# Performance work log

Measured on AMD Instinct MI355X. Metric: run time of the kernel, lower is better.

Reference implementation:

```python
import jax, jax.numpy as jnp
import numpy as np


def setup_inputs() -> dict:
    key = jax.random.key(0)
    k1, k2 = jax.random.split(key)
    B, D, C = 4096, 128, 64
    score = jax.random.normal(k1, (B, D), dtype=jnp.float32)
    target = jax.random.randint(k2, (B,), 0, C, dtype=jnp.int64)
    alpha = jnp.full((1,), 9.0, dtype=jnp.float32)  # learned margin param
    return {"score": score, "target": target, "alpha": alpha}


def _pairwise_dist(score):
    # squared euclidean: ||xi||^2 + ||xj||^2 - 2 xi.xj, clamped at 0, then sqrt
    mag = jnp.sum(score * score, axis=1)            # [B]
    d2 = mag[:, None] + mag[None, :] - 2.0 * (score @ score.T)
    d2 = jnp.maximum(d2, 0.0)
    # safe sqrt (diagonal is exactly 0; avoid nan grads)
    safe = jnp.where(d2 > 0.0, d2, 1.0)
    return jnp.where(d2 > 0.0, jnp.sqrt(safe), 0.0)  # [B, B]


def reference(score, target, alpha):
    target = target.reshape(-1)
    B = score.shape[0]
    dist = _pairwise_dist(score)                    # [B, B]
    diff = target[:, None] != target[None, :]       # [B, B] negative-pair mask
    # per-anchor sum over negatives of exp(alpha - dist); diagonal excluded (same label)
    nes = jnp.sum(jnp.where(diff, jnp.exp(alpha[0] - dist), 0.0), axis=1)  # [B]
    l_n = jnp.log(nes[:, None] + nes[None, :])      # [B, B]
    # positive pairs i<j with equal labels
    upper = jnp.triu(jnp.ones((B, B), dtype=bool), k=1)
    pos = (~diff) & upper
    terms = jnp.where(pos, jax.nn.relu(l_n + dist) ** 2, 0.0)
    counter = jnp.sum(pos).astype(score.dtype)
    return jnp.sum(terms) / (2.0 * counter)
```

## Files before the change

### kernel.cpp

```cpp
#include <hip/hip_runtime.h>
#include <math.h>

#define BN 4096
#define DD 128
#define NCLS 64
#define PSPLIT 16
#define NPOSB (NCLS * PSPLIT)
#define NJB 32

typedef __attribute__((ext_vector_type(8))) short short8;
typedef __attribute__((ext_vector_type(4))) float f32x4;

__device__ __forceinline__ unsigned short f2bf(float f) {
    unsigned int u = __float_as_uint(f);
    u += 0x7FFFu + ((u >> 16) & 1u);
    return (unsigned short)(u >> 16);
}

__device__ __forceinline__ void gload_lds16(const void* g, void* l) {
    __builtin_amdgcn_global_load_lds(
        (const __attribute__((address_space(1))) unsigned int*)g,
        (__attribute__((address_space(3))) unsigned int*)l, 16, 0, 0);
}


__global__ __launch_bounds__(256)
void prep_bucket_kernel(const float* __restrict__ score, const int* __restrict__ target,
                        unsigned short* __restrict__ sbf, float* __restrict__ mag,
                        int* __restrict__ cls_cnt, int* __restrict__ cls_start,
                        int* __restrict__ cls_list) {
    __shared__ int hist[NCLS];
    __shared__ int offs[NCLS];
    const int tid = threadIdx.x;
    if (blockIdx.x < BN / 4) {
        int row  = blockIdx.x * 4 + (tid >> 6);
        int lane = tid & 63;
        float2 v = *reinterpret_cast<const float2*>(score + (size_t)row * DD + lane * 2);
        float s = v.x * v.x + v.y * v.y;
        #pragma unroll
        for (int off = 32; off; off >>= 1) s += __shfl_xor(s, off);
        ushort2 u; u.x = f2bf(v.x); u.y = f2bf(v.y);
        *reinterpret_cast<ushort2*>(sbf + (size_t)row * DD + lane * 2) = u;
        if (lane == 0) mag[row] = s;
    } else {
        if (tid < NCLS) hist[tid] = 0;
        __syncthreads();
        for (int i = tid; i < BN; i += 256) atomicAdd(&hist[target[i]], 1);
        __syncthreads();
        if (tid == 0) {
            int run = 0;
            for (int c = 0; c < NCLS; ++c) {
                cls_cnt[c] = hist[c];
                cls_start[c] = run;
                offs[c] = run;
                run += hist[c];
            }
        }
        __syncthreads();
        for (int i = tid; i < BN; i += 256) {
            int p = atomicAdd(&offs[target[i]], 1);
            cls_list[p] = i;
        }
    }
}

__global__ __launch_bounds__(256)
void nes_kernel(const unsigned short* __restrict__ sbf, const int* __restrict__ target,
                const float* __restrict__ alphap, const float* __restrict__ mag,
                float* __restrict__ nes_part) {
    const int ib = blockIdx.x, jb = blockIdx.y;
    if (jb < ib) return;
    __shared__ __align__(16) unsigned short lds[2 * 128 * 128];
    __shared__ float rowsum[2][128];
    __shared__ float colsum[2][128];
    const int tid = threadIdx.x;
    const int w = tid >> 6, lane = tid & 63;
    const int lhi = lane >> 4, llo = lane & 15;
    const int i0 = ib * 128, j0 = jb * 128;
    const bool diag = (ib == jb);

    #pragma unroll
    for (int t = 0; t < 8; ++t) {
        int rl = w * 32 + t * 4 + lhi;
        int ch = llo ^ (rl & 7);
        gload_lds16(sbf + (size_t)(i0 + rl) * DD + ch * 8, lds + (w * 32 + t * 4) * 128);
        if (!diag)
            gload_lds16(sbf + (size_t)(j0 + rl) * DD + ch * 8,
                        lds + 128 * 128 + (w * 32 + t * 4) * 128);
    }
    __syncthreads();

    const unsigned short* bbase = diag ? lds : (lds + 128 * 128);
    const int wr = w >> 1, wc = w & 1;
    f32x4 acc[4][4] = {};
    #pragma unroll
    for (int kk = 0; kk < 4; ++kk) {
        short8 a[4], b[4];
        #pragma unroll
        for (int m = 0; m < 4; ++m) {
            int r = wr * 64 + m * 16 + llo;
            int ch = (kk * 4 + lhi) ^ (r & 7);
            a[m] = *reinterpret_cast<const short8*>(lds + r * 128 + ch * 8);
        }
        #pragma unroll
        for (int n = 0; n < 4; ++n) {
            int r = wc * 64 + n * 16 + llo;
            int ch = (kk * 4 + lhi) ^ (r & 7);
            b[n] = *reinterpret_cast<const short8*>(bbase + r * 128 + ch * 8);
        }
        #pragma unroll
        for (int m = 0; m < 4; ++m)
            #pragma unroll
            for (int n = 0; n < 4; ++n)
                acc[m][n] = __builtin_amdgcn_mfma_f32_16x16x32_bf16(a[m], b[n], acc[m][n], 0, 0, 0);
    }

    const float alpha = alphap[0];
    float mj[4]; int tj[4];
    #pragma unroll
    for (int n = 0; n < 4; ++n) {
        int j = j0 + wc * 64 + n * 16 + llo;
        mj[n] = mag[j]; tj[n] = target[j];
    }
    float cs[4] = {0.f, 0.f, 0.f, 0.f};
    #pragma unroll
    for (int m = 0; m < 4; ++m) {
        #pragma unroll
        for (int rg = 0; rg < 4; ++rg) {
            int li = wr * 64 + m * 16 + lhi * 4 + rg;
            int i = i0 + li;
            float mi = mag[i];
            int ti = target[i];
            float rs = 0.f;
            #pragma unroll
            for (int n = 0; n < 4; ++n) {
                float d2 = fmaxf(mi + mj[n] - 2.0f * acc[m][n][rg], 0.0f);
                float dist = sqrtf(d2);
                float e = (ti != tj[n]) ? __expf(alpha - dist) : 0.0f;
                rs += e;
                cs[n] += e;
            }
            rs += __shfl_xor(rs, 1);
            rs += __shfl_xor(rs, 2);
            rs += __shfl_xor(rs, 4);
            rs += __shfl_xor(rs, 8);
            if (llo == 0) rowsum[wc][li] = rs;
        }
    }
    #pragma unroll
    for (int n = 0; n < 4; ++n) {
        cs[n] += __shfl_xor(cs[n], 16);
        cs[n] += __shfl_xor(cs[n], 32);
        if (lhi == 0) colsum[wr][wc * 64 + n * 16 + llo] = cs[n];
    }
    __syncthreads();
    if (tid < 128) {
        nes_part[(size_t)(i0 + tid) * NJB + jb] = rowsum[0][tid] + rowsum[1][tid];
        if (!diag)
            nes_part[(size_t)(j0 + tid) * NJB + ib] = colsum[0][tid] + colsum[1][tid];
    }
}

__global__ __launch_bounds__(256)
void pos_kernel(const float* __restrict__ score, const float* __restrict__ nes_part,
                const int* __restrict__ cls_cnt, const int* __restrict__ cls_start,
                const int* __restrict__ cls_list,
                float* __restrict__ part_sum, unsigned int* __restrict__ part_cnt) {
    __shared__ float ssum[4];
    __shared__ unsigned int scnt[4];
    const int c = blockIdx.x;
    const int n = cls_cnt[c], s0 = cls_start[c];
    const int tid = threadIdx.x;
    const int grp = tid >> 4, llo = tid & 15;
    const int g0 = blockIdx.y * 16 + grp;
    const int nG = 16 * PSPLIT;
    const int nn = n * n;
    float s = 0.f;
    unsigned int cc = 0;
    for (int p = g0; p < nn; p += nG) {
        int a = p / n, b = p - a * n;
        if (b <= a) continue;
        int i = cls_list[s0 + a], j = cls_list[s0 + b];
        const float4* ra = reinterpret_cast<const float4*>(score + (size_t)i * DD) + llo * 2;
        const float4* rb = reinterpret_cast<const float4*>(score + (size_t)j * DD) + llo * 2;
        float4 x0 = ra[0], x1 = ra[1];
        float4 y0 = rb[0], y1 = rb[1];
        float dx;
        float d2 = 0.f;
        dx = x0.x - y0.x; d2 += dx * dx;
        dx = x0.y - y0.y; d2 += dx * dx;
        dx = x0.z - y0.z; d2 += dx * dx;
        dx = x0.w - y0.w; d2 += dx * dx;
        dx = x1.x - y1.x; d2 += dx * dx;
        dx = x1.y - y1.y; d2 += dx * dx;
        dx = x1.z - y1.z; d2 += dx * dx;
        dx = x1.w - y1.w; d2 += dx * dx;
        float2 pi = *reinterpret_cast<const float2*>(nes_part + (size_t)i * NJB + llo * 2);
        float2 pj = *reinterpret_cast<const float2*>(nes_part + (size_t)j * NJB + llo * 2);
        float ni = pi.x + pi.y;
        float nj = pj.x + pj.y;
        #pragma unroll
        for (int off = 1; off < 16; off <<= 1) {
            d2 += __shfl_xor(d2, off);
            ni += __shfl_xor(ni, off);
            nj += __shfl_xor(nj, off);
        }
        if (llo == 0) {
            float dist = sqrtf(d2);
            float t = __logf(ni + nj) + dist;
            if (t > 0.f) s += t * t;
            cc++;
        }
    }
    #pragma unroll
    for (int off = 1; off < 64; off <<= 1) {
        s += __shfl_xor(s, off);
        cc += __shfl_xor(cc, off);
    }
    if ((tid & 63) == 0) { ssum[tid >> 6] = s; scnt[tid >> 6] = cc; }
    __syncthreads();
    if (tid == 0) {
        int bid = blockIdx.y * NCLS + blockIdx.x;
        part_sum[bid] = ssum[0] + ssum[1] + ssum[2] + ssum[3];
        part_cnt[bid] = scnt[0] + scnt[1] + scnt[2] + scnt[3];
    }
}

__global__ __launch_bounds__(256)
void finalize_kernel(const float* __restrict__ part_sum,
                     const unsigned int* __restrict__ part_cnt,
                     float* __restrict__ out) {
    __shared__ float fs[4];
    __shared__ unsigned int fc[4];
    int tid = threadIdx.x;
    float s = 0.f;
    unsigned int c = 0;
    #pragma unroll
    for (int k = 0; k < NPOSB / 256; ++k) {
        s += part_sum[k * 256 + tid];
        c += part_cnt[k * 256 + tid];
    }
    #pragma unroll
    for (int off = 1; off < 64; off <<= 1) {
        s += __shfl_xor(s, off);
        c += __shfl_xor(c, off);
    }
    if ((tid & 63) == 0) { fs[tid >> 6] = s; fc[tid >> 6] = c; }
    __syncthreads();
    if (tid == 0) {
        float S = fs[0] + fs[1] + fs[2] + fs[3];
        float C = (float)(fc[0] + fc[1] + fc[2] + fc[3]);
        out[0] = S / (2.0f * C);
    }
}

extern "C" void kernel_launch(void* const* d_in, const int* in_sizes, int n_in,
                              void* d_out, int out_size, void* d_ws, size_t ws_size,
                              hipStream_t stream) {
    const float* score  = (const float*)d_in[0];
    const int*   target = (const int*)d_in[1];
    const float* alpha  = (const float*)d_in[2];
    float* out = (float*)d_out;

    unsigned short* sbf = (unsigned short*)d_ws;
    float* mag      = (float*)((char*)d_ws + (size_t)BN * DD * 2);
    float* nes_part = mag + BN;
    float* part_sum = nes_part + (size_t)BN * NJB;
    unsigned int* part_cnt = (unsigned int*)(part_sum + NPOSB);
    int* cls_cnt   = (int*)(part_cnt + NPOSB);
    int* cls_start = cls_cnt + NCLS;
    int* cls_list  = cls_start + NCLS;

    prep_bucket_kernel<<<BN / 4 + 1, 256, 0, stream>>>(score, target, sbf, mag,
                                                       cls_cnt, cls_start, cls_list);
    dim3 g(BN / 128, BN / 128);
    nes_kernel<<<g, 256, 0, stream>>>(sbf, target, alpha, mag, nes_part);
    pos_kernel<<<dim3(NCLS, PSPLIT), 256, 0, stream>>>(score, nes_part,
                                                       cls_cnt, cls_start, cls_list,
                                                       part_sum, part_cnt);
    finalize_kernel<<<1, 256, 0, stream>>>(part_sum, part_cnt, out);
}
```

Before: 109.8 us.

## Fuse all stages into one persistent kernel with grid-wide barriers

```diff
diff --git a/kernel.cpp b/kernel.cpp
--- a/kernel.cpp
+++ b/kernel.cpp
@@ -4,8 +4,9 @@
 #define BN 4096
 #define DD 128
 #define NCLS 64
-#define PSPLIT 16
-#define NPOSB (NCLS * PSPLIT)
+#define NT 32
+#define NTILES (NT * (NT + 1) / 2)
+#define NBLK 256
 #define NJB 32
 
 typedef __attribute__((ext_vector_type(8))) short short8;
@@ -23,234 +24,248 @@
         (__attribute__((address_space(3))) unsigned int*)l, 16, 0, 0);
 }
 
+__device__ __forceinline__ void grid_barrier(unsigned int* bar, int idx) {
+    __syncthreads();
+    if (threadIdx.x == 0) {
+        __threadfence();
+        atomicAdd(&bar[idx], 1u);
+        while (__hip_atomic_load(&bar[idx], __ATOMIC_ACQUIRE, __HIP_MEMORY_SCOPE_AGENT) < NBLK)
+            __builtin_amdgcn_s_sleep(2);
+    }
+    __syncthreads();
+    __threadfence();
+}
+
 
 __global__ __launch_bounds__(256)
-void prep_bucket_kernel(const float* __restrict__ score, const int* __restrict__ target,
-                        unsigned short* __restrict__ sbf, float* __restrict__ mag,
-                        int* __restrict__ cls_cnt, int* __restrict__ cls_start,
-                        int* __restrict__ cls_list) {
-    __shared__ int hist[NCLS];
-    __shared__ int offs[NCLS];
-    const int tid = threadIdx.x;
-    if (blockIdx.x < BN / 4) {
-        int row  = blockIdx.x * 4 + (tid >> 6);
-        int lane = tid & 63;
-        float2 v = *reinterpret_cast<const float2*>(score + (size_t)row * DD + lane * 2);
-        float s = v.x * v.x + v.y * v.y;
-        #pragma unroll
-        for (int off = 32; off; off >>= 1) s += __shfl_xor(s, off);
-        ushort2 u; u.x = f2bf(v.x); u.y = f2bf(v.y);
-        *reinterpret_cast<ushort2*>(sbf + (size_t)row * DD + lane * 2) = u;
-        if (lane == 0) mag[row] = s;
-    } else {
-        if (tid < NCLS) hist[tid] = 0;
-        __syncthreads();
-        for (int i = tid; i < BN; i += 256) atomicAdd(&hist[target[i]], 1);
-        __syncthreads();
-        if (tid == 0) {
-            int run = 0;
-            for (int c = 0; c < NCLS; ++c) {
-                cls_cnt[c] = hist[c];
-                cls_start[c] = run;
-                offs[c] = run;
-                run += hist[c];
-            }
-        }
-        __syncthreads();
-        for (int i = tid; i < BN; i += 256) {
-            int p = atomicAdd(&offs[target[i]], 1);
-            cls_list[p] = i;
-        }
-    }
-}
-
-__global__ __launch_bounds__(256)
-void nes_kernel(const unsigned short* __restrict__ sbf, const int* __restrict__ target,
-                const float* __restrict__ alphap, const float* __restrict__ mag,
-                float* __restrict__ nes_part) {
-    const int ib = blockIdx.x, jb = blockIdx.y;
-    if (jb < ib) return;
+void mega_kernel(const float* __restrict__ score, const int* __restrict__ target,
+                 const float* __restrict__ alphap, float* __restrict__ out,
+                 unsigned int* __restrict__ bar,
+                 unsigned short* __restrict__ sbf, float* __restrict__ mag,
+                 float* __restrict__ nes_part,
+                 float* __restrict__ part_sum, unsigned int* __restrict__ part_cnt,
+                 int* __restrict__ cls_cnt, int* __restrict__ cls_start,
+                 int* __restrict__ cls_list) {
     __shared__ __align__(16) unsigned short lds[2 * 128 * 128];
     __shared__ float rowsum[2][128];
     __shared__ float colsum[2][128];
-    const int tid = threadIdx.x;
-    const int w = tid >> 6, lane = tid & 63;
-    const int lhi = lane >> 4, llo = lane & 15;
-    const int i0 = ib * 128, j0 = jb * 128;
-    const bool diag = (ib == jb);
-
-    #pragma unroll
-    for (int t = 0; t < 8; ++t) {
-        int rl = w * 32 + t * 4 + lhi;
-        int ch = llo ^ (rl & 7);
-        gload_lds16(sbf + (size_t)(i0 + rl) * DD + ch * 8, lds + (w * 32 + t * 4) * 128);
-        if (!diag)
-            gload_lds16(sbf + (size_t)(j0 + rl) * DD + ch * 8,
-                        lds + 128 * 128 + (w * 32 + t * 4) * 128);
-    }
-    __syncthreads();
-
-    const unsigned short* bbase = diag ? lds : (lds + 128 * 128);
-    const int wr = w >> 1, wc = w & 1;
-    f32x4 acc[4][4] = {};
-    #pragma unroll
-    for (int kk = 0; kk < 4; ++kk) {
-        short8 a[4], b[4];
-        #pragma unroll
-        for (int m = 0; m < 4; ++m) {
-            int r = wr * 64 + m * 16 + llo;
-            int ch = (kk * 4 + lhi) ^ (r & 7);
-            a[m] = *reinterpret_cast<const short8*>(lds + r * 128 + ch * 8);
-        }
-        #pragma unroll
-        for (int n = 0; n < 4; ++n) {
-            int r = wc * 64 + n * 16 + llo;
-            int ch = (kk * 4 + lhi) ^ (r & 7);
-            b[n] = *reinterpret_cast<const short8*>(bbase + r * 128 + ch * 8);
-        }
-        #pragma unroll
-        for (int m = 0; m < 4; ++m)
-            #pragma unroll
-            for (int n = 0; n < 4; ++n)
-                acc[m][n] = __builtin_amdgcn_mfma_f32_16x16x32_bf16(a[m], b[n], acc[m][n], 0, 0, 0);
-    }
-
-    const float alpha = alphap[0];
-    float mj[4]; int tj[4];
-    #pragma unroll
-    for (int n = 0; n < 4; ++n) {
-        int j = j0 + wc * 64 + n * 16 + llo;
-        mj[n] = mag[j]; tj[n] = target[j];
-    }
-    float cs[4] = {0.f, 0.f, 0.f, 0.f};
-    #pragma unroll
-    for (int m = 0; m < 4; ++m) {
-        #pragma unroll
-        for (int rg = 0; rg < 4; ++rg) {
-            int li = wr * 64 + m * 16 + lhi * 4 + rg;
-            int i = i0 + li;
-            float mi = mag[i];
-            int ti = target[i];
-            float rs = 0.f;
-            #pragma unroll
-            for (int n = 0; n < 4; ++n) {
-                float d2 = fmaxf(mi + mj[n] - 2.0f * acc[m][n][rg], 0.0f);
-                float dist = sqrtf(d2);
-                float e = (ti != tj[n]) ? __expf(alpha - dist) : 0.0f;
-                rs += e;
-                cs[n] += e;
-            }
-            rs += __shfl_xor(rs, 1);
-            rs += __shfl_xor(rs, 2);
-            rs += __shfl_xor(rs, 4);
-            rs += __shfl_xor(rs, 8);
-            if (llo == 0) rowsum[wc][li] = rs;
-        }
-    }
-    #pragma unroll
-    for (int n = 0; n < 4; ++n) {
-        cs[n] += __shfl_xor(cs[n], 16);
-        cs[n] += __shfl_xor(cs[n], 32);
-        if (lhi == 0) colsum[wr][wc * 64 + n * 16 + llo] = cs[n];
-    }
-    __syncthreads();
-    if (tid < 128) {
-        nes_part[(size_t)(i0 + tid) * NJB + jb] = rowsum[0][tid] + rowsum[1][tid];
-        if (!diag)
-            nes_part[(size_t)(j0 + tid) * NJB + ib] = colsum[0][tid] + colsum[1][tid];
-    }
-}
-
-__global__ __launch_bounds__(256)
-void pos_kernel(const float* __restrict__ score, const float* __restrict__ nes_part,
-                const int* __restrict__ cls_cnt, const int* __restrict__ cls_start,
-                const int* __restrict__ cls_list,
-                float* __restrict__ part_sum, unsigned int* __restrict__ part_cnt) {
     __shared__ float ssum[4];
     __shared__ unsigned int scnt[4];
-    const int c = blockIdx.x;
-    const int n = cls_cnt[c], s0 = cls_start[c];
+
+    const int b   = blockIdx.x;
     const int tid = threadIdx.x;
-    const int grp = tid >> 4, llo = tid & 15;
-    const int g0 = blockIdx.y * 16 + grp;
-    const int nG = 16 * PSPLIT;
-    const int nn = n * n;
-    float s = 0.f;
-    unsigned int cc = 0;
-    for (int p = g0; p < nn; p += nG) {
-        int a = p / n, b = p - a * n;
-        if (b <= a) continue;
-        int i = cls_list[s0 + a], j = cls_list[s0 + b];
-        const float4* ra = reinterpret_cast<const float4*>(score + (size_t)i * DD) + llo * 2;
-        const float4* rb = reinterpret_cast<const float4*>(score + (size_t)j * DD) + llo * 2;
-        float4 x0 = ra[0], x1 = ra[1];
-        float4 y0 = rb[0], y1 = rb[1];
-        float dx;
-        float d2 = 0.f;
-        dx = x0.x - y0.x; d2 += dx * dx;
-        dx = x0.y - y0.y; d2 += dx * dx;
-        dx = x0.z - y0.z; d2 += dx * dx;
-        dx = x0.w - y0.w; d2 += dx * dx;
-        dx = x1.x - y1.x; d2 += dx * dx;
-        dx = x1.y - y1.y; d2 += dx * dx;
-        dx = x1.z - y1.z; d2 += dx * dx;
-        dx = x1.w - y1.w; d2 += dx * dx;
-        float2 pi = *reinterpret_cast<const float2*>(nes_part + (size_t)i * NJB + llo * 2);
-        float2 pj = *reinterpret_cast<const float2*>(nes_part + (size_t)j * NJB + llo * 2);
-        float ni = pi.x + pi.y;
-        float nj = pj.x + pj.y;
+    const int lane = tid & 63;
+    const int lhi = lane >> 4, llo = lane & 15;
+    const int w = tid >> 6;
+
+    {
         #pragma unroll
-        for (int off = 1; off < 16; off <<= 1) {
-            d2 += __shfl_xor(d2, off);
-            ni += __shfl_xor(ni, off);
-            nj += __shfl_xor(nj, off);
-        }
-        if (llo == 0) {
-            float dist = sqrtf(d2);
-            float t = __logf(ni + nj) + dist;
-            if (t > 0.f) s += t * t;
-            cc++;
-        }
-    }
-    #pragma unroll
-    for (int off = 1; off < 64; off <<= 1) {
-        s += __shfl_xor(s, off);
-        cc += __shfl_xor(cc, off);
-    }
-    if ((tid & 63) == 0) { ssum[tid >> 6] = s; scnt[tid >> 6] = cc; }
-    __syncthreads();
-    if (tid == 0) {
-        int bid = blockIdx.y * NCLS + blockIdx.x;
-        part_sum[bid] = ssum[0] + ssum[1] + ssum[2] + ssum[3];
-        part_cnt[bid] = scnt[0] + scnt[1] + scnt[2] + scnt[3];
-    }
-}
-
-__global__ __launch_bounds__(256)
-void finalize_kernel(const float* __restrict__ part_sum,
-                     const unsigned int* __restrict__ part_cnt,
-                     float* __restrict__ out) {
-    __shared__ float fs[4];
-    __shared__ unsigned int fc[4];
-    int tid = threadIdx.x;
-    float s = 0.f;
-    unsigned int c = 0;
-    #pragma unroll
-    for (int k = 0; k < NPOSB / 256; ++k) {
-        s += part_sum[k * 256 + tid];
-        c += part_cnt[k * 256 + tid];
-    }
-    #pragma unroll
-    for (int off = 1; off < 64; off <<= 1) {
-        s += __shfl_xor(s, off);
-        c += __shfl_xor(c, off);
-    }
-    if ((tid & 63) == 0) { fs[tid >> 6] = s; fc[tid >> 6] = c; }
-    __syncthreads();
-    if (tid == 0) {
-        float S = fs[0] + fs[1] + fs[2] + fs[3];
-        float C = (float)(fc[0] + fc[1] + fc[2] + fc[3]);
-        out[0] = S / (2.0f * C);
+        for (int it = 0; it < 4; ++it) {
+            int row = (b * 4 + it) * 4 + w;
+            float2 v = *reinterpret_cast<const float2*>(score + (size_t)row * DD + lane * 2);
+            float s = v.x * v.x + v.y * v.y;
+            #pragma unroll
+            for (int off = 32; off; off >>= 1) s += __shfl_xor(s, off);
+            ushort2 u; u.x = f2bf(v.x); u.y = f2bf(v.y);
+            *reinterpret_cast<ushort2*>(sbf + (size_t)row * DD + lane * 2) = u;
+            if (lane == 0) mag[row] = s;
+        }
+        if (b == NBLK - 1) {
+            int* hist = reinterpret_cast<int*>(lds);
+            int* offs = hist + NCLS;
+            if (tid < NCLS) hist[tid] = 0;
+            __syncthreads();
+            for (int i = tid; i < BN; i += 256) atomicAdd(&hist[target[i]], 1);
+            __syncthreads();
+            if (tid == 0) {
+                int run = 0;
+                for (int c = 0; c < NCLS; ++c) {
+                    cls_cnt[c] = hist[c];
+                    cls_start[c] = run;
+                    offs[c] = run;
+                    run += hist[c];
+                }
+            }
+            __syncthreads();
+            for (int i = tid; i < BN; i += 256) {
+                int p = atomicAdd(&offs[target[i]], 1);
+                cls_list[p] = i;
+            }
+        }
+    }
+    grid_barrier(bar, 0);
+
+    {
+        const float alpha = alphap[0];
+        const int wr = w >> 1, wc = w & 1;
+        bool first = true;
+        for (int t = b; t < NTILES; t += NBLK) {
+            int ib = 0, rem = t;
+            while (rem >= NT - ib) { rem -= NT - ib; ib++; }
+            int jb = ib + rem;
+            const int i0 = ib * 128, j0 = jb * 128;
+            const bool diag = (ib == jb);
+
+            if (!first) __syncthreads();
+            first = false;
+            #pragma unroll
+            for (int tt = 0; tt < 8; ++tt) {
+                int rl = w * 32 + tt * 4 + lhi;
+                int ch = llo ^ (rl & 7);
+                gload_lds16(sbf + (size_t)(i0 + rl) * DD + ch * 8,
+                            lds + (w * 32 + tt * 4) * 128);
+                if (!diag)
+                    gload_lds16(sbf + (size_t)(j0 + rl) * DD + ch * 8,
+                                lds + 128 * 128 + (w * 32 + tt * 4) * 128);
+            }
+            __syncthreads();
+
+            const unsigned short* bbase = diag ? lds : (lds + 128 * 128);
+            f32x4 acc[4][4] = {};
+            #pragma unroll
+            for (int kk = 0; kk < 4; ++kk) {
+                short8 a[4], bb[4];
+                #pragma unroll
+                for (int m = 0; m < 4; ++m) {
+                    int r = wr * 64 + m * 16 + llo;
+                    int ch = (kk * 4 + lhi) ^ (r & 7);
+                    a[m] = *reinterpret_cast<const short8*>(lds + r * 128 + ch * 8);
+                }
+                #pragma unroll
+                for (int n = 0; n < 4; ++n) {
+                    int r = wc * 64 + n * 16 + llo;
+                    int ch = (kk * 4 + lhi) ^ (r & 7);
+                    bb[n] = *reinterpret_cast<const short8*>(bbase + r * 128 + ch * 8);
+                }
+                #pragma unroll
+                for (int m = 0; m < 4; ++m)
+                    #pragma unroll
+                    for (int n = 0; n < 4; ++n)
+                        acc[m][n] = __builtin_amdgcn_mfma_f32_16x16x32_bf16(a[m], bb[n], acc[m][n], 0, 0, 0);
+            }
+
+            float mj[4]; int tj[4];
+            #pragma unroll
+            for (int n = 0; n < 4; ++n) {
+                int j = j0 + wc * 64 + n * 16 + llo;
+                mj[n] = mag[j]; tj[n] = target[j];
+            }
+            float cs[4] = {0.f, 0.f, 0.f, 0.f};
+            #pragma unroll
+            for (int m = 0; m < 4; ++m) {
+                #pragma unroll
+                for (int rg = 0; rg < 4; ++rg) {
+                    int li = wr * 64 + m * 16 + lhi * 4 + rg;
+                    int i = i0 + li;
+                    float mi = mag[i];
+                    int ti = target[i];
+                    float rs = 0.f;
+                    #pragma unroll
+                    for (int n = 0; n < 4; ++n) {
+                        float d2 = fmaxf(mi + mj[n] - 2.0f * acc[m][n][rg], 0.0f);
+                        float dist = sqrtf(d2);
+                        float e = (ti != tj[n]) ? __expf(alpha - dist) : 0.0f;
+                        rs += e;
+                        cs[n] += e;
+                    }
+                    rs += __shfl_xor(rs, 1);
+                    rs += __shfl_xor(rs, 2);
+                    rs += __shfl_xor(rs, 4);
+                    rs += __shfl_xor(rs, 8);
+                    if (llo == 0) rowsum[wc][li] = rs;
+                }
+            }
+            #pragma unroll
+            for (int n = 0; n < 4; ++n) {
+                cs[n] += __shfl_xor(cs[n], 16);
+                cs[n] += __shfl_xor(cs[n], 32);
+                if (lhi == 0) colsum[wr][wc * 64 + n * 16 + llo] = cs[n];
+            }
+            __syncthreads();
+            if (tid < 128) {
+                nes_part[(size_t)(i0 + tid) * NJB + jb] = rowsum[0][tid] + rowsum[1][tid];
+                if (!diag)
+                    nes_part[(size_t)(j0 + tid) * NJB + ib] = colsum[0][tid] + colsum[1][tid];
+            }
+        }
+    }
+    grid_barrier(bar, 1);
+
+    {
+        const int c  = b & 63;
+        const int sp = b >> 6;
+        const int n = cls_cnt[c], s0 = cls_start[c];
+        const int grp = tid >> 4;
+        const int g0 = sp * 16 + grp;
+        const int nG = 64;
+        const int nn = n * n;
+        float s = 0.f;
+        unsigned int cc = 0;
+        for (int p = g0; p < nn; p += nG) {
+            int a = p / n, bq = p - a * n;
+            if (bq <= a) continue;
+            int i = cls_list[s0 + a], j = cls_list[s0 + bq];
+            const float4* ra = reinterpret_cast<const float4*>(score + (size_t)i * DD) + llo * 2;
+            const float4* rb = reinterpret_cast<const float4*>(score + (size_t)j * DD) + llo * 2;
+            float4 x0 = ra[0], x1 = ra[1];
+            float4 y0 = rb[0], y1 = rb[1];
+            float dx, d2 = 0.f;
+            dx = x0.x - y0.x; d2 += dx * dx;
+            dx = x0.y - y0.y; d2 += dx * dx;
+            dx = x0.z - y0.z; d2 += dx * dx;
+            dx = x0.w - y0.w; d2 += dx * dx;
+            dx = x1.x - y1.x; d2 += dx * dx;
+            dx = x1.y - y1.y; d2 += dx * dx;
+            dx = x1.z - y1.z; d2 += dx * dx;
+            dx = x1.w - y1.w; d2 += dx * dx;
+            float2 pi = *reinterpret_cast<const float2*>(nes_part + (size_t)i * NJB + llo * 2);
+            float2 pj = *reinterpret_cast<const float2*>(nes_part + (size_t)j * NJB + llo * 2);
+            float ni = pi.x + pi.y;
+            float nj = pj.x + pj.y;
+            #pragma unroll
+            for (int off = 1; off < 16; off <<= 1) {
+                d2 += __shfl_xor(d2, off);
+                ni += __shfl_xor(ni, off);
+                nj += __shfl_xor(nj, off);
+            }
+            if (llo == 0) {
+                float dist = sqrtf(d2);
+                float tv = __logf(ni + nj) + dist;
+                if (tv > 0.f) s += tv * tv;
+                cc++;
+            }
+        }
+        #pragma unroll
+        for (int off = 1; off < 64; off <<= 1) {
+            s += __shfl_xor(s, off);
+            cc += __shfl_xor(cc, off);
+        }
+        __syncthreads();
+        if ((tid & 63) == 0) { ssum[w] = s; scnt[w] = cc; }
+        __syncthreads();
+        if (tid == 0) {
+            part_sum[b] = ssum[0] + ssum[1] + ssum[2] + ssum[3];
+            part_cnt[b] = scnt[0] + scnt[1] + scnt[2] + scnt[3];
+        }
+    }
+    grid_barrier(bar, 2);
+
+    if (b == 0) {
+        float s = part_sum[tid];
+        unsigned int c = part_cnt[tid];
+        #pragma unroll
+        for (int off = 1; off < 64; off <<= 1) {
+            s += __shfl_xor(s, off);
+            c += __shfl_xor(c, off);
+        }
+        __syncthreads();
+        if ((tid & 63) == 0) { ssum[w] = s; scnt[w] = c; }
+        __syncthreads();
+        if (tid == 0) {
+            float S = ssum[0] + ssum[1] + ssum[2] + ssum[3];
+            float C = (float)(scnt[0] + scnt[1] + scnt[2] + scnt[3]);
+            out[0] = S / (2.0f * C);
+        }
     }
 }
 
@@ -262,21 +277,19 @@
     const float* alpha  = (const float*)d_in[2];
     float* out = (float*)d_out;
 
-    unsigned short* sbf = (unsigned short*)d_ws;
-    float* mag      = (float*)((char*)d_ws + (size_t)BN * DD * 2);
+    unsigned int* bar = (unsigned int*)d_ws;
+    unsigned short* sbf = (unsigned short*)(bar + 8);
+    float* mag      = (float*)((char*)sbf + (size_t)BN * DD * 2);
     float* nes_part = mag + BN;
     float* part_sum = nes_part + (size_t)BN * NJB;
-    unsigned int* part_cnt = (unsigned int*)(part_sum + NPOSB);
-    int* cls_cnt   = (int*)(part_cnt + NPOSB);
+    unsigned int* part_cnt = (unsigned int*)(part_sum + NBLK);
+    int* cls_cnt   = (int*)(part_cnt + NBLK);
     int* cls_start = cls_cnt + NCLS;
     int* cls_list  = cls_start + NCLS;
 
-    prep_bucket_kernel<<<BN / 4 + 1, 256, 0, stream>>>(score, target, sbf, mag,
-                                                       cls_cnt, cls_start, cls_list);
-    dim3 g(BN / 128, BN / 128);
-    nes_kernel<<<g, 256, 0, stream>>>(sbf, target, alpha, mag, nes_part);
-    pos_kernel<<<dim3(NCLS, PSPLIT), 256, 0, stream>>>(score, nes_part,
-                                                       cls_cnt, cls_start, cls_list,
-                                                       part_sum, part_cnt);
-    finalize_kernel<<<1, 256, 0, stream>>>(part_sum, part_cnt, out);
-}
+    hipMemsetAsync(bar, 0, 8 * sizeof(unsigned int), stream);
+    mega_kernel<<<NBLK, 256, 0, stream>>>(score, target, alpha, out,
+                                          bar, sbf, mag, nes_part,
+                                          part_sum, part_cnt,
+                                          cls_cnt, cls_start, cls_list);
+}
```

Result: slower. 323.8 us (+194.9%).
